# Kernel tuning notes

Hardware: AMD Instinct MI355X
Metric: run time of the kernel (lower is better)

The kernel has to match this reference:

```python
import jax, jax.numpy as jnp
import numpy as np
from itertools import product as iter_product

N_QUBITS = 6
DIM = 2 ** N_QUBITS            # 64
N_GEN = DIM * DIM - 1          # 4095
DEPTH = 4
N_OBS = 15

_GENS = None

def _build_generators(n):
    I = np.eye(2, dtype=np.complex64)
    X = np.array([[0, 1], [1, 0]], np.complex64)
    Y = np.array([[0, -1j], [1j, 0]], np.complex64)
    Z = np.array([[1, 0], [0, -1]], np.complex64)
    P = [I, X, Y, Z]
    gens = []
    for idx in iter_product(range(4), repeat=n):
        if all(i == 0 for i in idx):
            continue
        m = P[idx[0]]
        for k in range(1, n):
            m = np.kron(m, P[idx[k]])
        gens.append(m)
    return jnp.asarray(np.stack(gens))  # [4^n-1, 2^n, 2^n] complex64

def _gens():
    global _GENS
    if _GENS is None:
        _GENS = _build_generators(N_QUBITS)
    return _GENS

def _apply_ry(psi, q, theta, n):
    # psi: [B, 2^n] complex; RY(theta) on qubit q
    B = psi.shape[0]
    x = psi.reshape(B, 2 ** q, 2, 2 ** (n - q - 1))
    c = jnp.cos(theta / 2)
    s = jnp.sin(theta / 2)
    s0, s1 = x[:, :, 0, :], x[:, :, 1, :]
    x = jnp.stack([c * s0 - s * s1, s * s0 + c * s1], axis=2)
    return x.reshape(B, -1)

def _apply_cnot(psi, c, t, n):
    # psi: [B, 2^n]; CNOT control c, target t
    B = psi.shape[0]
    x = psi.reshape((B,) + (2,) * n)
    ax_c, ax_t = 1 + c, 1 + t
    x0 = jnp.take(x, 0, axis=ax_c)
    x1 = jnp.take(x, 1, axis=ax_c)
    ax_t2 = ax_t - (1 if ax_t > ax_c else 0)
    x1 = jnp.flip(x1, axis=ax_t2)
    x = jnp.stack([x0, x1], axis=ax_c)
    return x.reshape(B, -1)

def _make_hermitians(A, B, D):
    # create_Hermitian vectorized over the m observables.
    # h[i,j] = A[idx]+iB[idx] for j<i (row-major lower-tri), h[i-1,i-1]=D[i];
    # then H = h + h^H.
    il, jl = jnp.tril_indices(DIM, -1)  # row-major order matches count+j loop
    di = jnp.arange(DIM - 1)

    def one(a, b, d):
        h = jnp.zeros((DIM, DIM), jnp.complex64)
        h = h.at[il, jl].set(a + 1j * b)
        h = h.at[di, di].set(d[1:].astype(jnp.complex64))
        return h + h.conj().T

    return jax.vmap(one)(A, B, D)  # [m, DIM, DIM]

def setup_inputs() -> dict:
    key = jax.random.key(0)
    ks = jax.random.split(key, 8)
    batch, input_dim, hidden = 256, 1024, 2047
    n_off = DIM * (DIM - 1) // 2  # 2016
    return {
        "x": jax.random.normal(ks[0], (batch, input_dim), jnp.float32),
        "W1": 0.02 * jax.random.normal(ks[1], (input_dim, hidden), jnp.float32),
        "b1": jnp.zeros((hidden,), jnp.float32),
        "W2": 0.02 * jax.random.normal(ks[2], (hidden, N_GEN), jnp.float32),
        "b2": jnp.zeros((N_GEN,), jnp.float32),
        "var_params": 0.01 * jax.random.normal(ks[3], (DEPTH, N_QUBITS), jnp.float32),
        "A": 2.0 * jax.random.normal(ks[4], (N_OBS, n_off), jnp.float32),
        "B": 2.0 * jax.random.normal(ks[5], (N_OBS, n_off), jnp.float32),
        "D": 2.0 * jax.random.normal(ks[6], (N_OBS, DIM), jnp.float32),
    }

def reference(x, W1, b1, W2, b2, var_params, A, B, D):
    n = N_QUBITS
    # encoding projection: Linear -> SiLU -> Linear
    h = jax.nn.silu(x @ W1 + b1)
    theta = h @ W2 + b2  # [batch, 4^n - 1]
    gens = _gens()  # [n_gen, dim, dim] complex64 (constant)
    # A_mat = sum_g theta_g G_g (Hermitian), U = exp(i A_mat)
    Amat = jnp.einsum('bg,gij->bij', theta.astype(jnp.complex64), gens)
    U = jax.vmap(jax.scipy.linalg.expm)(1j * Amat)  # [batch, dim, dim]
    psi = U[:, :, 0]  # apply to |0...0>
    # hardware-efficient VQC: RY layer + CNOT ring per depth
    for d in range(DEPTH):
        for q in range(n):
            psi = _apply_ry(psi, q, var_params[d, q], n)
        for q in range(n):
            psi = _apply_cnot(psi, q, (q + 1) % n, n)
    H = _make_hermitians(A, B, D)  # [m, dim, dim]
    # expectation <psi|H_w|psi>
    exp = jnp.einsum('bi,wij,bj->bw', psi.conj(), H, psi).real
    return exp  # [batch, n_observables]
```

## Files before the change

### kernel.cpp

```cpp
#include <hip/hip_runtime.h>
#include <math.h>

typedef unsigned short ushort_t;
typedef __attribute__((ext_vector_type(8))) short bf16x8_t;
typedef __attribute__((ext_vector_type(4))) float f32x4_t;

__device__ __forceinline__ void tsplit(float v, unsigned& h, unsigned& l) {
  unsigned u = __float_as_uint(v);
  h = u >> 16;
  float lo = v - __uint_as_float(u & 0xffff0000u);
  l = __float_as_uint(lo) >> 16;
}

__device__ __forceinline__ void transpose_tile(
    const float* __restrict__ W, ushort_t* __restrict__ Wh,
    ushort_t* __restrict__ Wl, int K, int N, int Kpad, int n0, int k0, int t) {
  __shared__ float sh[32][33];
  const int tx = t & 31, ty = t >> 5;
#pragma unroll
  for (int i = 0; i < 4; ++i) {
    int k = k0 + i * 8 + ty;
    float v = (k < K && (n0 + tx) < N) ? W[(size_t)k * N + n0 + tx] : 0.f;
    sh[tx][i * 8 + ty] = v;
  }
  __syncthreads();
  const int nn = t >> 3;
  const int kq = t & 7;
  unsigned h[4], l[4];
#pragma unroll
  for (int e = 0; e < 4; ++e) tsplit(sh[nn][kq * 4 + e], h[e], l[e]);
  size_t o = (size_t)(n0 + nn) * Kpad + k0 + kq * 4;
  uint2 ph, pl;
  ph.x = h[0] | (h[1] << 16); ph.y = h[2] | (h[3] << 16);
  pl.x = l[0] | (l[1] << 16); pl.y = l[2] | (l[3] << 16);
  *(uint2*)&Wh[o] = ph;
  *(uint2*)&Wl[o] = pl;
}

__global__ __launch_bounds__(256) void prep2_kernel(
    const float* __restrict__ x, const float* __restrict__ W1,
    ushort_t* __restrict__ xh, ushort_t* __restrict__ xl,
    ushort_t* __restrict__ w1h, ushort_t* __restrict__ w1l) {
  const int bid = blockIdx.x;
  const int t = threadIdx.x;
  if (bid < 256) {
    int i4 = bid * 256 + t;
    float4 v = ((const float4*)x)[i4];
    unsigned h0, l0, h1, l1, h2, l2, h3, l3;
    tsplit(v.x, h0, l0); tsplit(v.y, h1, l1);
    tsplit(v.z, h2, l2); tsplit(v.w, h3, l3);
    uint2 ph, pl;
    ph.x = h0 | (h1 << 16); ph.y = h2 | (h3 << 16);
    pl.x = l0 | (l1 << 16); pl.y = l2 | (l3 << 16);
    ((uint2*)xh)[i4] = ph;
    ((uint2*)xl)[i4] = pl;
  } else {
    int tau = bid - 256;
    transpose_tile(W1, w1h, w1l, 1024, 2047, 1024,
                   (tau & 63) * 32, (tau >> 6) * 32, t);
  }
}

#define LSTR 40

__global__ __launch_bounds__(256) void gemm1_w2t_kernel(
    const ushort_t* __restrict__ xh, const ushort_t* __restrict__ xl,
    const ushort_t* __restrict__ w1h, const ushort_t* __restrict__ w1l,
    const float* __restrict__ b1,
    ushort_t* __restrict__ hh, ushort_t* __restrict__ hl,
    const float* __restrict__ W2,
    ushort_t* __restrict__ w2h, ushort_t* __restrict__ w2l) {
  const int bid = blockIdx.x;
  const int t = threadIdx.x;
  if (bid >= 256) {
    int tau = bid - 256;
    transpose_tile(W2, w2h, w2l, 2047, 4095, 2048,
                   (tau & 127) * 32, (tau >> 7) * 32, t);
    return;
  }
  __shared__ ushort_t As[2][32 * LSTR];
  __shared__ ushort_t Bs[2][64 * LSTR];
  const int lane = t & 63;
  const int wv = t >> 6;
  const int l15 = lane & 15;
  const int quad = lane >> 4;
  const int m0 = (bid >> 5) * 32;
  const int n0 = (bid & 31) * 64;

  f32x4_t acc[2];
  acc[0] = (f32x4_t){0.f, 0.f, 0.f, 0.f};
  acc[1] = (f32x4_t){0.f, 0.f, 0.f, 0.f};

  for (int k0 = 0; k0 < 1024; k0 += 32) {
    if (wv < 2) {
      const ushort_t* src = wv ? xl : xh;
      ushort_t* dst = As[wv];
#pragma unroll
      for (int q = 0; q < 2; ++q) {
        int r = q * 16 + (lane >> 2);
        int c = (lane & 3) * 8;
        *(int4*)&dst[r * LSTR + c] =
            *(const int4*)(src + (size_t)(m0 + r) * 1024 + k0 + c);
      }
    } else {
      const ushort_t* src = (wv == 3) ? w1l : w1h;
      ushort_t* dst = Bs[wv - 2];
#pragma unroll
      for (int q = 0; q < 4; ++q) {
        int r = q * 16 + (lane >> 2);
        int c = (lane & 3) * 8;
        *(int4*)&dst[r * LSTR + c] =
            *(const int4*)(src + (size_t)(n0 + r) * 1024 + k0 + c);
      }
    }
    __syncthreads();
    bf16x8_t bfh = *(const bf16x8_t*)&Bs[0][(wv * 16 + l15) * LSTR + quad * 8];
    bf16x8_t bfl = *(const bf16x8_t*)&Bs[1][(wv * 16 + l15) * LSTR + quad * 8];
#pragma unroll
    for (int i = 0; i < 2; ++i) {
      int mr = i * 16 + l15;
      bf16x8_t afh = *(const bf16x8_t*)&As[0][mr * LSTR + quad * 8];
      bf16x8_t afl = *(const bf16x8_t*)&As[1][mr * LSTR + quad * 8];
      acc[i] = __builtin_amdgcn_mfma_f32_16x16x32_bf16(afh, bfh, acc[i], 0, 0, 0);
      acc[i] = __builtin_amdgcn_mfma_f32_16x16x32_bf16(afh, bfl, acc[i], 0, 0, 0);
      acc[i] = __builtin_amdgcn_mfma_f32_16x16x32_bf16(afl, bfh, acc[i], 0, 0, 0);
    }
    __syncthreads();
  }
#pragma unroll
  for (int i = 0; i < 2; ++i) {
    int col = n0 + wv * 16 + l15;
#pragma unroll
    for (int rg = 0; rg < 4; ++rg) {
      int row = m0 + i * 16 + quad * 4 + rg;
      float v = acc[i][rg];
      if (col < 2047) {
        v += b1[col];
        v = v / (1.f + expf(-v));
      } else {
        v = 0.f;
      }
      unsigned h, l;
      tsplit(v, h, l);
      size_t o = (size_t)row * 2048 + col;
      hh[o] = (ushort_t)h;
      hl[o] = (ushort_t)l;
    }
  }
}

__global__ __launch_bounds__(256) void gemm2k_kernel(
    const ushort_t* __restrict__ Ah, const ushort_t* __restrict__ Al,
    const ushort_t* __restrict__ Bh, const ushort_t* __restrict__ Bl,
    float* __restrict__ part) {
  __shared__ ushort_t Ab[2][128 * LSTR];
  __shared__ ushort_t Bb[2][64 * LSTR];
  const int t = threadIdx.x;
  const int lane = t & 63;
  const int wv = t >> 6;
  const int l15 = lane & 15;
  const int quad = lane >> 4;
  const int wm = wv >> 1, wn = wv & 1;
  const int m0 = blockIdx.y * 128;
  const int n0 = blockIdx.x * 64;
  const int ks = blockIdx.z;

  f32x4_t acc[4][2];
#pragma unroll
  for (int i = 0; i < 4; ++i)
#pragma unroll
    for (int j = 0; j < 2; ++j) acc[i][j] = (f32x4_t){0.f, 0.f, 0.f, 0.f};

  for (int kt = 0; kt < 16; ++kt) {
    const int k0 = ks * 512 + kt * 32;
    if (wv < 2) {
      const ushort_t* src = wv ? Al : Ah;
      ushort_t* dst = Ab[wv];
#pragma unroll
      for (int q = 0; q < 8; ++q) {
        int r = q * 16 + (lane >> 2);
        int c = (lane & 3) * 8;
        *(int4*)&dst[r * LSTR + c] =
            *(const int4*)(src + (size_t)(m0 + r) * 2048 + k0 + c);
      }
    } else {
      const ushort_t* src = (wv == 3) ? Bl : Bh;
      ushort_t* dst = Bb[wv - 2];
#pragma unroll
      for (int q = 0; q < 4; ++q) {
        int r = q * 16 + (lane >> 2);
        int c = (lane & 3) * 8;
        *(int4*)&dst[r * LSTR + c] =
            *(const int4*)(src + (size_t)(n0 + r) * 2048 + k0 + c);
      }
    }
    __syncthreads();
    bf16x8_t bfh[2], bfl[2];
#pragma unroll
    for (int j = 0; j < 2; ++j) {
      int nr = wn * 32 + j * 16 + l15;
      bfh[j] = *(const bf16x8_t*)&Bb[0][nr * LSTR + quad * 8];
      bfl[j] = *(const bf16x8_t*)&Bb[1][nr * LSTR + quad * 8];
    }
#pragma unroll
    for (int i = 0; i < 4; ++i) {
      int mr = wm * 64 + i * 16 + l15;
      bf16x8_t afh = *(const bf16x8_t*)&Ab[0][mr * LSTR + quad * 8];
      bf16x8_t afl = *(const bf16x8_t*)&Ab[1][mr * LSTR + quad * 8];
#pragma unroll
      for (int j = 0; j < 2; ++j) {
        acc[i][j] = __builtin_amdgcn_mfma_f32_16x16x32_bf16(
            afh, bfh[j], acc[i][j], 0, 0, 0);
        acc[i][j] = __builtin_amdgcn_mfma_f32_16x16x32_bf16(
            afh, bfl[j], acc[i][j], 0, 0, 0);
        acc[i][j] = __builtin_amdgcn_mfma_f32_16x16x32_bf16(
            afl, bfh[j], acc[i][j], 0, 0, 0);
      }
    }
    __syncthreads();
  }
  float* pbase = part + (size_t)ks * 256 * 4096;
#pragma unroll
  for (int i = 0; i < 4; ++i)
#pragma unroll
    for (int j = 0; j < 2; ++j) {
      int row0 = m0 + wm * 64 + i * 16 + quad * 4;
      int col = n0 + wn * 32 + j * 16 + l15;
#pragma unroll
      for (int rg = 0; rg < 4; ++rg)
        pbase[(size_t)(row0 + rg) * 4096 + col] = acc[i][j][rg];
    }
}

#define TM 64
#define TN 64
#define TK 16
__global__ __launch_bounds__(256) void gemm_tiled(
    const float* __restrict__ X, const float* __restrict__ W,
    const float* __restrict__ bias, float* __restrict__ out,
    int M, int N, int K, int ldx, int ldw, int ldo, int doSilu, int padN)
{
  __shared__ float Xs[TK][TM + 4];
  __shared__ float Ws[TK][TN + 4];
  const int t = threadIdx.x;
  const int n0 = blockIdx.x * TN;
  const int m0 = blockIdx.y * TM;
  const int tr = t >> 4, tc = t & 15;
  float acc[4][4];
#pragma unroll
  for (int i = 0; i < 4; ++i)
#pragma unroll
    for (int j = 0; j < 4; ++j) acc[i][j] = 0.f;
  const int xr = t >> 2, xk = (t & 3) * 4;
  const int wk = t >> 4, wc = (t & 15) * 4;
  for (int k0 = 0; k0 < K; k0 += TK) {
    {
      const float* xp = X + (size_t)(m0 + xr) * ldx + (k0 + xk);
      float xv[4];
      if (k0 + xk + 3 < K) {
        float4 v = *(const float4*)xp;
        xv[0] = v.x; xv[1] = v.y; xv[2] = v.z; xv[3] = v.w;
      } else {
#pragma unroll
        for (int e = 0; e < 4; ++e) xv[e] = (k0 + xk + e < K) ? xp[e] : 0.f;
      }
#pragma unroll
      for (int e = 0; e < 4; ++e) Xs[xk + e][xr] = xv[e];
    }
    {
      const int kk = k0 + wk;
      const float* wp = W + (size_t)kk * ldw + (n0 + wc);
      const bool kv = kk < K;
#pragma unroll
      for (int e = 0; e < 4; ++e) {
        int n = n0 + wc + e;
        Ws[wk][wc + e] = (kv && n < N) ? wp[e] : 0.f;
      }
    }
    __syncthreads();
#pragma unroll
    for (int k = 0; k < TK; ++k) {
      float4 av = *(const float4*)&Xs[k][tr * 4];
      float4 bv = *(const float4*)&Ws[k][tc * 4];
      float a4[4] = {av.x, av.y, av.z, av.w};
      float b4[4] = {bv.x, bv.y, bv.z, bv.w};
#pragma unroll
      for (int i = 0; i < 4; ++i)
#pragma unroll
        for (int j = 0; j < 4; ++j)
          acc[i][j] = fmaf(a4[i], b4[j], acc[i][j]);
    }
    __syncthreads();
  }
#pragma unroll
  for (int i = 0; i < 4; ++i) {
    const int mrow = m0 + tr * 4 + i;
    float* op = out + (size_t)mrow * ldo;
#pragma unroll
    for (int j = 0; j < 4; ++j) {
      const int n = n0 + tc * 4 + j;
      if (n < N) {
        float v = acc[i][j] + bias[n];
        if (doSilu) v = v / (1.f + expf(-v));
        op[n] = v;
      } else if (n < padN) {
        op[n] = 0.f;
      }
    }
  }
}

#define RS 72
#define PL (64 * RS)

__device__ __forceinline__ void qmm4(
    const ushort_t* __restrict__ Prm, const ushort_t* __restrict__ Qcm,
    float* ore, float* oim, int mt, int nt, int quad, int l15)
{
  f32x4_t aR = (f32x4_t){0.f, 0.f, 0.f, 0.f};
  f32x4_t aN = (f32x4_t){0.f, 0.f, 0.f, 0.f};
  f32x4_t aI = (f32x4_t){0.f, 0.f, 0.f, 0.f};
#pragma unroll
  for (int kb = 0; kb < 2; ++kb) {
    const int ko = kb * 32 + quad * 8;
    const int ra = (mt * 16 + l15) * RS + ko;
    bf16x8_t arh = *(const bf16x8_t*)&Prm[0 * PL + ra];
    bf16x8_t arl = *(const bf16x8_t*)&Prm[1 * PL + ra];
    bf16x8_t aih = *(const bf16x8_t*)&Prm[2 * PL + ra];
    bf16x8_t ail = *(const bf16x8_t*)&Prm[3 * PL + ra];
    const int rb = (nt * 16 + l15) * RS + ko;
    bf16x8_t brh = *(const bf16x8_t*)&Qcm[0 * PL + rb];
    bf16x8_t brl = *(const bf16x8_t*)&Qcm[1 * PL + rb];
    bf16x8_t bih = *(const bf16x8_t*)&Qcm[2 * PL + rb];
    bf16x8_t bil = *(const bf16x8_t*)&Qcm[3 * PL + rb];
    aR = __builtin_amdgcn_mfma_f32_16x16x32_bf16(arh, brh, aR, 0, 0, 0);
    aR = __builtin_amdgcn_mfma_f32_16x16x32_bf16(arh, brl, aR, 0, 0, 0);
    aR = __builtin_amdgcn_mfma_f32_16x16x32_bf16(arl, brh, aR, 0, 0, 0);
    aN = __builtin_amdgcn_mfma_f32_16x16x32_bf16(aih, bih, aN, 0, 0, 0);
    aN = __builtin_amdgcn_mfma_f32_16x16x32_bf16(aih, bil, aN, 0, 0, 0);
    aN = __builtin_amdgcn_mfma_f32_16x16x32_bf16(ail, bih, aN, 0, 0, 0);
    aI = __builtin_amdgcn_mfma_f32_16x16x32_bf16(arh, bih, aI, 0, 0, 0);
    aI = __builtin_amdgcn_mfma_f32_16x16x32_bf16(arh, bil, aI, 0, 0, 0);
    aI = __builtin_amdgcn_mfma_f32_16x16x32_bf16(arl, bih, aI, 0, 0, 0);
    aI = __builtin_amdgcn_mfma_f32_16x16x32_bf16(aih, brh, aI, 0, 0, 0);
    aI = __builtin_amdgcn_mfma_f32_16x16x32_bf16(aih, brl, aI, 0, 0, 0);
    aI = __builtin_amdgcn_mfma_f32_16x16x32_bf16(ail, brh, aI, 0, 0, 0);
  }
#pragma unroll
  for (int rg = 0; rg < 4; ++rg) {
    ore[rg] = aR[rg] - aN[rg];
    oim[rg] = aI[rg];
  }
}

__device__ __forceinline__ void stage_rm4(
    ushort_t* rm, const float* re, const float* im, int mt, int nt,
    int quad, int l15)
{
  unsigned rh[4], rl[4], ih[4], il[4];
#pragma unroll
  for (int rg = 0; rg < 4; ++rg) {
    tsplit(re[rg], rh[rg], rl[rg]);
    tsplit(im[rg], ih[rg], il[rg]);
  }
#pragma unroll
  for (int rg = 0; rg < 4; ++rg) {
    int idx = (mt * 16 + quad * 4 + rg) * RS + nt * 16 + l15;
    rm[0 * PL + idx] = (ushort_t)rh[rg];
    rm[1 * PL + idx] = (ushort_t)rl[rg];
    rm[2 * PL + idx] = (ushort_t)ih[rg];
    rm[3 * PL + idx] = (ushort_t)il[rg];
  }
}

__device__ __forceinline__ void stage_cm4(
    ushort_t* cm, const float* re, const float* im, int mt, int nt,
    int quad, int l15)
{
  unsigned rh[4], rl[4], ih[4], il[4];
#pragma unroll
  for (int rg = 0; rg < 4; ++rg) {
    tsplit(re[rg], rh[rg], rl[rg]);
    tsplit(im[rg], ih[rg], il[rg]);
  }
  int base = (nt * 16 + l15) * RS + mt * 16 + quad * 4;
  uint2 p;
  p.x = rh[0] | (rh[1] << 16); p.y = rh[2] | (rh[3] << 16);
  *(uint2*)&cm[0 * PL + base] = p;
  p.x = rl[0] | (rl[1] << 16); p.y = rl[2] | (rl[3] << 16);
  *(uint2*)&cm[1 * PL + base] = p;
  p.x = ih[0] | (ih[1] << 16); p.y = ih[2] | (ih[3] << 16);
  *(uint2*)&cm[2 * PL + base] = p;
  p.x = il[0] | (il[1] << 16); p.y = il[2] | (il[3] << 16);
  *(uint2*)&cm[3 * PL + base] = p;
}

__device__ __forceinline__ void stage_both4(
    ushort_t* rm, ushort_t* cm, const float* re, const float* im,
    int mt, int nt, int quad, int l15)
{
  stage_rm4(rm, re, im, mt, nt, quad, l15);
  stage_cm4(cm, re, im, mt, nt, quad, l15);
}

__global__ __launch_bounds__(1024, 4) void quantum_kernel(
    const float* __restrict__ pin,
    const float* __restrict__ b2g,
    const float* __restrict__ vp,
    const float* __restrict__ Aobs,
    const float* __restrict__ Bobs,
    const float* __restrict__ Dobs,
    float* __restrict__ out,
    int fused)
{
  __shared__ __align__(16) ushort_t PQ[2][8 * PL];
  __shared__ float ps[128];
  __shared__ float scr16[16];
  __shared__ float csb[24], snb[24];
  __shared__ float sAf;
  __shared__ int   sS;

  float*  thetas = (float*)&PQ[1][0];
  float2* Als    = (float2*)&PQ[0][0];

  const int t = threadIdx.x;
  const int b = blockIdx.x;
  const int lane = t & 63;
  const int w = t >> 6;
  const int quad = lane >> 4;
  const int l15 = lane & 15;
  const int mt = w >> 2, nt = w & 3;

  float ssq;
  {
    float4 v = ((const float4*)(pin + (size_t)b * 4096))[t];
    if (fused) {
#pragma unroll
      for (int k = 1; k < 4; ++k) {
        float4 u =
            ((const float4*)(pin + (size_t)k * 256 * 4096 + (size_t)b * 4096))[t];
        v.x += u.x; v.y += u.y; v.z += u.z; v.w += u.w;
      }
      int n0i = 4 * t;
      v.x += b2g[n0i];
      v.y += b2g[n0i + 1];
      v.z += b2g[n0i + 2];
      if (n0i + 3 < 4095) v.w += b2g[n0i + 3];
    }
    if (t == 1023) v.w = 0.f;
    thetas[4 * t + 0] = v.x; thetas[4 * t + 1] = v.y;
    thetas[4 * t + 2] = v.z; thetas[4 * t + 3] = v.w;
    ssq = v.x * v.x + v.y * v.y + v.z * v.z + v.w * v.w;
  }
#pragma unroll
  for (int mm = 1; mm < 64; mm <<= 1) ssq += __shfl_xor(ssq, mm);
  if (lane == 0) scr16[w] = ssq;
  __syncthreads();
  if (w == 0) {
    float s = (lane < 16) ? scr16[lane] : 0.f;
#pragma unroll
    for (int mm = 1; mm < 64; mm <<= 1) s += __shfl_xor(s, mm);
    if (lane == 0) {
      float frob = fmaxf(8.f * sqrtf(s), 1e-3f);
      sAf = frob;
      float bound = 0.30f * frob;
      int sc = (bound > 1.f) ? (int)ceilf(log2f(bound)) : 0;
      sS = sc < 0 ? 0 : (sc > 12 ? 12 : sc);
    }
  } else if (w == 1 && lane < 24) {
    float sn, cs;
    sincosf(vp[lane] * 0.5f, &sn, &cs);
    snb[lane] = sn;
    csb[lane] = cs;
  }
  __syncthreads();
  const int sPow = sS;

  for (int xx = 0; xx < 4; ++xx) {
    const int x = w + 16 * xx;
    const int z = lane;
    int g1 = 0;
#pragma unroll
    for (int bq = 0; bq < 6; ++bq) {
      int xb = (x >> bq) & 1, zb = (z >> bq) & 1;
      int dig = xb ? (zb ? 2 : 1) : (zb ? 3 : 0);
      g1 |= dig << (2 * bq);
    }
    float tv = (g1 == 0) ? 0.f : thetas[g1 - 1];
    int pc = __popc(x & z) & 3;
    float re, im;
    switch (pc) {
      case 0:  re = tv;  im = 0.f;  break;
      case 1:  re = 0.f; im = -tv;  break;
      case 2:  re = -tv; im = 0.f;  break;
      default: re = 0.f; im = tv;   break;
    }
#pragma unroll
    for (int mk = 1; mk < 64; mk <<= 1) {
      float ore = __shfl_xor(re, mk);
      float oim = __shfl_xor(im, mk);
      if (z & mk) { re = ore - re; im = oim - im; }
      else        { re = re + ore; im = im + oim; }
    }
    Als[z * 66 + (z ^ x)] = make_float2(re, im);
  }
  __syncthreads();

  const float scl = ldexpf(1.f, -sPow);
  float bre[4], bim[4];
#pragma unroll
  for (int rg = 0; rg < 4; ++rg) {
    int row = mt * 16 + quad * 4 + rg;
    int col = nt * 16 + l15;
    float2 v = Als[row * 66 + col];
    bre[rg] = -v.y * scl;
    bim[rg] =  v.x * scl;
  }
  __syncthreads();

  ushort_t* b0 = &PQ[0][0];
  ushort_t* b1 = &PQ[1][0];
  stage_both4(b0, b0 + 4 * PL, bre, bim, mt, nt, quad, l15);
  __syncthreads();
  float b2re[4], b2im[4];
  qmm4(b0, b0 + 4 * PL, b2re, b2im, mt, nt, quad, l15);
  stage_both4(b1, b1 + 4 * PL, b2re, b2im, mt, nt, quad, l15);
  __syncthreads();
  float b3re[4], b3im[4];
  qmm4(b1, b0 + 4 * PL, b3re, b3im, mt, nt, quad, l15);

  const float c3 = 1.f / 6.f, c4 = 1.f / 24.f, c5 = 1.f / 120.f;
  const float c6 = 1.f / 720.f, c7 = 1.f / 5040.f, c8 = 1.f / 40320.f;
  float s1re[4], s1im[4], p0re[4], p0im[4];
#pragma unroll
  for (int rg = 0; rg < 4; ++rg) {
    float dg = (mt == nt && l15 == quad * 4 + rg) ? 1.f : 0.f;
    s1re[rg] = c4 * dg + c5 * bre[rg] + c6 * b2re[rg] + c7 * b3re[rg];
    s1im[rg] =           c5 * bim[rg] + c6 * b2im[rg] + c7 * b3im[rg];
    p0re[rg] = dg + bre[rg] + 0.5f * b2re[rg] + c3 * b3re[rg];
    p0im[rg] =      bim[rg] + 0.5f * b2im[rg] + c3 * b3im[rg];
  }
  float b4re[4], b4im[4];
  qmm4(b1, b1 + 4 * PL, b4re, b4im, mt, nt, quad, l15);
#pragma unroll
  for (int rg = 0; rg < 4; ++rg) {
    s1re[rg] += c8 * b4re[rg];
    s1im[rg] += c8 * b4im[rg];
  }
  __syncthreads();
  stage_rm4(b0, s1re, s1im, mt, nt, quad, l15);
  stage_cm4(b0 + 4 * PL, b4re, b4im, mt, nt, quad, l15);
  __syncthreads();
  float ure[4], uim[4];
  qmm4(b0, b0 + 4 * PL, ure, uim, mt, nt, quad, l15);
#pragma unroll
  for (int rg = 0; rg < 4; ++rg) {
    ure[rg] += p0re[rg];
    uim[rg] += p0im[rg];
  }

  int cur = 1;
  for (int q = 0; q < sPow; ++q) {
    ushort_t* bb = &PQ[cur][0];
    stage_both4(bb, bb + 4 * PL, ure, uim, mt, nt, quad, l15);
    __syncthreads();
    qmm4(bb, bb + 4 * PL, ure, uim, mt, nt, quad, l15);
    cur ^= 1;
  }

  if (nt == 0 && l15 == 0) {
#pragma unroll
    for (int rg = 0; rg < 4; ++rg) {
      int row = mt * 16 + quad * 4 + rg;
      ps[2 * row] = ure[rg];
      ps[2 * row + 1] = uim[rg];
    }
  }
  __syncthreads();

  if (t < 64) {
    float pre = ps[2 * t], pim = ps[2 * t + 1];
#pragma unroll
    for (int d = 0; d < 4; ++d) {
#pragma unroll
      for (int q = 0; q < 6; ++q) {
        float s = snb[d * 6 + q], c = csb[d * 6 + q];
        int bpos = 5 - q;
        int bit = (t >> bpos) & 1;
        float ore = __shfl_xor(pre, 1 << bpos);
        float oim = __shfl_xor(pim, 1 << bpos);
        float sg = bit ? s : -s;
        pre = c * pre + sg * ore;
        pim = c * pim + sg * oim;
      }
#pragma unroll
      for (int q = 0; q < 6; ++q) {
        int bc = 5 - q;
        int bt = 5 - ((q + 1) % 6);
        float ore = __shfl_xor(pre, 1 << bt);
        float oim = __shfl_xor(pim, 1 << bt);
        int ctrl = (t >> bc) & 1;
        pre = ctrl ? ore : pre;
        pim = ctrl ? oim : pim;
      }
    }
    ps[2 * t] = pre; ps[2 * t + 1] = pim;
  }
  __syncthreads();

  float* Rt = (float*)&PQ[0][0];
  float* It = Rt + 2016;
  for (int p = t; p < 2016; p += 1024) {
    int i = (int)((1.f + sqrtf(8.f * (float)p + 1.f)) * 0.5f);
    while (i * (i - 1) / 2 > p) --i;
    while (i * (i + 1) / 2 <= p) ++i;
    int j = p - i * (i - 1) / 2;
    float pri = ps[2 * i], pii = ps[2 * i + 1];
    float prj = ps[2 * j], pij = ps[2 * j + 1];
    Rt[p] = pri * prj + pii * pij;
    It[p] = pri * pij - pii * prj;
  }
  __syncthreads();

  if (w < 15) {
    float xr = ps[2 * lane], xi = ps[2 * lane + 1];
    float mypsq = xr * xr + xi * xi;
    const float* Ap = Aobs + w * 2016;
    const float* Bp = Bobs + w * 2016;
    float part = 0.f;
    for (int p2 = lane; p2 < 1008; p2 += 64) {
      float2 a = *(const float2*)&Ap[2 * p2];
      float2 bb2 = *(const float2*)&Bp[2 * p2];
      float2 rt = *(const float2*)&Rt[2 * p2];
      float2 it = *(const float2*)&It[2 * p2];
      part += a.x * rt.x - bb2.x * it.x;
      part += a.y * rt.y - bb2.y * it.y;
    }
    if (lane < 63) part += Dobs[w * 64 + lane + 1] * mypsq;
#pragma unroll
    for (int mm = 1; mm < 64; mm <<= 1) part += __shfl_xor(part, mm);
    if (lane == 0) out[b * 15 + w] = 2.f * part;
  }
}

extern "C" void kernel_launch(void* const* d_in, const int* in_sizes, int n_in,
                              void* d_out, int out_size, void* d_ws, size_t ws_size,
                              hipStream_t stream) {
  const float* x  = (const float*)d_in[0];
  const float* W1 = (const float*)d_in[1];
  const float* b1 = (const float*)d_in[2];
  const float* W2 = (const float*)d_in[3];
  const float* b2 = (const float*)d_in[4];
  const float* vp = (const float*)d_in[5];
  const float* Ao = (const float*)d_in[6];
  const float* Bo = (const float*)d_in[7];
  const float* Do = (const float*)d_in[8];
  float* out = (float*)d_out;

  const size_t O_XH  = 0;
  const size_t O_XL  = 524288;
  const size_t O_W1H = 1048576;
  const size_t O_W1L = 5242880;
  const size_t O_PT  = 0;
  const size_t O_W2H = 16777216;
  const size_t O_W2L = 33554432;
  const size_t O_HH  = 50331648;
  const size_t O_HL  = 51380224;
  const size_t NEED  = 52428800;

  if (ws_size >= NEED) {
    char* ws = (char*)d_ws;
    ushort_t* xh  = (ushort_t*)(ws + O_XH);
    ushort_t* xl  = (ushort_t*)(ws + O_XL);
    ushort_t* w1h = (ushort_t*)(ws + O_W1H);
    ushort_t* w1l = (ushort_t*)(ws + O_W1L);
    float* part16 = (float*)(ws + O_PT);
    ushort_t* w2h = (ushort_t*)(ws + O_W2H);
    ushort_t* w2l = (ushort_t*)(ws + O_W2L);
    ushort_t* hh  = (ushort_t*)(ws + O_HH);
    ushort_t* hl  = (ushort_t*)(ws + O_HL);

    prep2_kernel<<<2304, 256, 0, stream>>>(x, W1, xh, xl, w1h, w1l);
    gemm1_w2t_kernel<<<8448, 256, 0, stream>>>(
        xh, xl, w1h, w1l, b1, hh, hl, W2, w2h, w2l);
    gemm2k_kernel<<<dim3(64, 2, 4), 256, 0, stream>>>(hh, hl, w2h, w2l, part16);
    quantum_kernel<<<256, 1024, 0, stream>>>(part16, b2, vp, Ao, Bo, Do, out, 1);
  } else {
    float* h     = (float*)d_ws;
    float* theta = h + 256 * 2048;
    gemm_tiled<<<dim3(32, 4), 256, 0, stream>>>(
        x, W1, b1, h, 256, 2047, 1024, 1024, 2047, 2048, 1, 2048);
    gemm_tiled<<<dim3(64, 4), 256, 0, stream>>>(
        h, W2, b2, theta, 256, 4095, 2047, 2048, 4095, 4096, 0, 4096);
    quantum_kernel<<<256, 1024, 0, stream>>>(theta, b2, vp, Ao, Bo, Do, out, 0);
  }
}
```

Before: 173.9 us.

## Fuse fp32-to-bf16 hi/lo splitting into GEMM tile loads, drop prep transposes

The separate prep pass and the W2 transpose pass are removed. Both GEMMs now read fp32 x, W1 and W2 directly and split them into bf16 hi/lo pairs while staging tiles in shared memory. This cuts a kernel launch and the round trip of writing and re-reading large transposed weight copies in the workspace. In exchange, the weight loads in the GEMM loops become strided column reads (one float per thread per row), which may be poorly coalesced, and each gemm2 block repeats the split work that was previously done once.

```diff
diff --git a/kernel.cpp b/kernel.cpp
--- a/kernel.cpp
+++ b/kernel.cpp
@@ -12,149 +12,104 @@
   l = __float_as_uint(lo) >> 16;
 }
 
-__device__ __forceinline__ void transpose_tile(
-    const float* __restrict__ W, ushort_t* __restrict__ Wh,
-    ushort_t* __restrict__ Wl, int K, int N, int Kpad, int n0, int k0, int t) {
-  __shared__ float sh[32][33];
-  const int tx = t & 31, ty = t >> 5;
-#pragma unroll
-  for (int i = 0; i < 4; ++i) {
-    int k = k0 + i * 8 + ty;
-    float v = (k < K && (n0 + tx) < N) ? W[(size_t)k * N + n0 + tx] : 0.f;
-    sh[tx][i * 8 + ty] = v;
-  }
-  __syncthreads();
-  const int nn = t >> 3;
-  const int kq = t & 7;
-  unsigned h[4], l[4];
-#pragma unroll
-  for (int e = 0; e < 4; ++e) tsplit(sh[nn][kq * 4 + e], h[e], l[e]);
-  size_t o = (size_t)(n0 + nn) * Kpad + k0 + kq * 4;
-  uint2 ph, pl;
-  ph.x = h[0] | (h[1] << 16); ph.y = h[2] | (h[3] << 16);
-  pl.x = l[0] | (l[1] << 16); pl.y = l[2] | (l[3] << 16);
-  *(uint2*)&Wh[o] = ph;
-  *(uint2*)&Wl[o] = pl;
-}
-
-__global__ __launch_bounds__(256) void prep2_kernel(
+__device__ __forceinline__ void split8(const float* p, bf16x8_t& hi, bf16x8_t& lo) {
+#pragma unroll
+  for (int e = 0; e < 8; ++e) {
+    unsigned h, l;
+    tsplit(p[e], h, l);
+    hi[e] = (short)h;
+    lo[e] = (short)l;
+  }
+}
+
+#define LSTR 40
+
+__global__ __launch_bounds__(512) void gemm1_kernel(
     const float* __restrict__ x, const float* __restrict__ W1,
-    ushort_t* __restrict__ xh, ushort_t* __restrict__ xl,
-    ushort_t* __restrict__ w1h, ushort_t* __restrict__ w1l) {
-  const int bid = blockIdx.x;
+    const float* __restrict__ b1,
+    ushort_t* __restrict__ hh, ushort_t* __restrict__ hl) {
+  __shared__ __align__(16) ushort_t As[2][32 * LSTR];
+  __shared__ __align__(16) ushort_t Bs[2][64 * LSTR];
   const int t = threadIdx.x;
-  if (bid < 256) {
-    int i4 = bid * 256 + t;
-    float4 v = ((const float4*)x)[i4];
-    unsigned h0, l0, h1, l1, h2, l2, h3, l3;
-    tsplit(v.x, h0, l0); tsplit(v.y, h1, l1);
-    tsplit(v.z, h2, l2); tsplit(v.w, h3, l3);
-    uint2 ph, pl;
-    ph.x = h0 | (h1 << 16); ph.y = h2 | (h3 << 16);
-    pl.x = l0 | (l1 << 16); pl.y = l2 | (l3 << 16);
-    ((uint2*)xh)[i4] = ph;
-    ((uint2*)xl)[i4] = pl;
-  } else {
-    int tau = bid - 256;
-    transpose_tile(W1, w1h, w1l, 1024, 2047, 1024,
-                   (tau & 63) * 32, (tau >> 6) * 32, t);
-  }
-}
-
-#define LSTR 40
-
-__global__ __launch_bounds__(256) void gemm1_w2t_kernel(
-    const ushort_t* __restrict__ xh, const ushort_t* __restrict__ xl,
-    const ushort_t* __restrict__ w1h, const ushort_t* __restrict__ w1l,
-    const float* __restrict__ b1,
-    ushort_t* __restrict__ hh, ushort_t* __restrict__ hl,
-    const float* __restrict__ W2,
-    ushort_t* __restrict__ w2h, ushort_t* __restrict__ w2l) {
-  const int bid = blockIdx.x;
-  const int t = threadIdx.x;
-  if (bid >= 256) {
-    int tau = bid - 256;
-    transpose_tile(W2, w2h, w2l, 2047, 4095, 2048,
-                   (tau & 127) * 32, (tau >> 7) * 32, t);
-    return;
-  }
-  __shared__ ushort_t As[2][32 * LSTR];
-  __shared__ ushort_t Bs[2][64 * LSTR];
   const int lane = t & 63;
   const int wv = t >> 6;
   const int l15 = lane & 15;
   const int quad = lane >> 4;
-  const int m0 = (bid >> 5) * 32;
-  const int n0 = (bid & 31) * 64;
-
-  f32x4_t acc[2];
-  acc[0] = (f32x4_t){0.f, 0.f, 0.f, 0.f};
-  acc[1] = (f32x4_t){0.f, 0.f, 0.f, 0.f};
+  const int wm = wv & 1;
+  const int wn = wv >> 1;
+  const int m0 = (blockIdx.x >> 5) * 32;
+  const int n0 = (blockIdx.x & 31) * 64;
+
+  f32x4_t acc = (f32x4_t){0.f, 0.f, 0.f, 0.f};
+
+  const int xrow = (t & 127) >> 2;
+  const int xkq  = (t & 3) * 8;
+  const int wu   = t - 128;
+  const int wnx  = wu & 63;
+  const int wkh  = (wu >> 6) & 3;
+  const bool wok = (n0 + wnx) < 2047;
 
   for (int k0 = 0; k0 < 1024; k0 += 32) {
-    if (wv < 2) {
-      const ushort_t* src = wv ? xl : xh;
-      ushort_t* dst = As[wv];
-#pragma unroll
-      for (int q = 0; q < 2; ++q) {
-        int r = q * 16 + (lane >> 2);
-        int c = (lane & 3) * 8;
-        *(int4*)&dst[r * LSTR + c] =
-            *(const int4*)(src + (size_t)(m0 + r) * 1024 + k0 + c);
-      }
+    if (t < 128) {
+      const float* src = x + (size_t)(m0 + xrow) * 1024 + k0 + xkq;
+      float p[8];
+      float4 va = *(const float4*)src;
+      float4 vb = *(const float4*)(src + 4);
+      p[0] = va.x; p[1] = va.y; p[2] = va.z; p[3] = va.w;
+      p[4] = vb.x; p[5] = vb.y; p[6] = vb.z; p[7] = vb.w;
+      bf16x8_t hi, lo;
+      split8(p, hi, lo);
+      *(bf16x8_t*)&As[0][xrow * LSTR + xkq] = hi;
+      *(bf16x8_t*)&As[1][xrow * LSTR + xkq] = lo;
+    } else if (t < 384) {
+      float p[8];
+#pragma unroll
+      for (int i = 0; i < 8; ++i) {
+        int k = k0 + wkh * 8 + i;
+        p[i] = wok ? W1[(size_t)k * 2047 + n0 + wnx] : 0.f;
+      }
+      bf16x8_t hi, lo;
+      split8(p, hi, lo);
+      *(bf16x8_t*)&Bs[0][wnx * LSTR + wkh * 8] = hi;
+      *(bf16x8_t*)&Bs[1][wnx * LSTR + wkh * 8] = lo;
+    }
+    __syncthreads();
+    const int nr = wn * 16 + l15;
+    bf16x8_t bfh = *(const bf16x8_t*)&Bs[0][nr * LSTR + quad * 8];
+    bf16x8_t bfl = *(const bf16x8_t*)&Bs[1][nr * LSTR + quad * 8];
+    const int mr = wm * 16 + l15;
+    bf16x8_t afh = *(const bf16x8_t*)&As[0][mr * LSTR + quad * 8];
+    bf16x8_t afl = *(const bf16x8_t*)&As[1][mr * LSTR + quad * 8];
+    acc = __builtin_amdgcn_mfma_f32_16x16x32_bf16(afh, bfh, acc, 0, 0, 0);
+    acc = __builtin_amdgcn_mfma_f32_16x16x32_bf16(afh, bfl, acc, 0, 0, 0);
+    acc = __builtin_amdgcn_mfma_f32_16x16x32_bf16(afl, bfh, acc, 0, 0, 0);
+    __syncthreads();
+  }
+  const int col = n0 + wn * 16 + l15;
+#pragma unroll
+  for (int rg = 0; rg < 4; ++rg) {
+    int row = m0 + wm * 16 + quad * 4 + rg;
+    float v = acc[rg];
+    if (col < 2047) {
+      v += b1[col];
+      v = v / (1.f + expf(-v));
     } else {
-      const ushort_t* src = (wv == 3) ? w1l : w1h;
-      ushort_t* dst = Bs[wv - 2];
-#pragma unroll
-      for (int q = 0; q < 4; ++q) {
-        int r = q * 16 + (lane >> 2);
-        int c = (lane & 3) * 8;
-        *(int4*)&dst[r * LSTR + c] =
-            *(const int4*)(src + (size_t)(n0 + r) * 1024 + k0 + c);
-      }
-    }
-    __syncthreads();
-    bf16x8_t bfh = *(const bf16x8_t*)&Bs[0][(wv * 16 + l15) * LSTR + quad * 8];
-    bf16x8_t bfl = *(const bf16x8_t*)&Bs[1][(wv * 16 + l15) * LSTR + quad * 8];
-#pragma unroll
-    for (int i = 0; i < 2; ++i) {
-      int mr = i * 16 + l15;
-      bf16x8_t afh = *(const bf16x8_t*)&As[0][mr * LSTR + quad * 8];
-      bf16x8_t afl = *(const bf16x8_t*)&As[1][mr * LSTR + quad * 8];
-      acc[i] = __builtin_amdgcn_mfma_f32_16x16x32_bf16(afh, bfh, acc[i], 0, 0, 0);
-      acc[i] = __builtin_amdgcn_mfma_f32_16x16x32_bf16(afh, bfl, acc[i], 0, 0, 0);
-      acc[i] = __builtin_amdgcn_mfma_f32_16x16x32_bf16(afl, bfh, acc[i], 0, 0, 0);
-    }
-    __syncthreads();
-  }
-#pragma unroll
-  for (int i = 0; i < 2; ++i) {
-    int col = n0 + wv * 16 + l15;
-#pragma unroll
-    for (int rg = 0; rg < 4; ++rg) {
-      int row = m0 + i * 16 + quad * 4 + rg;
-      float v = acc[i][rg];
-      if (col < 2047) {
-        v += b1[col];
-        v = v / (1.f + expf(-v));
-      } else {
-        v = 0.f;
-      }
-      unsigned h, l;
-      tsplit(v, h, l);
-      size_t o = (size_t)row * 2048 + col;
-      hh[o] = (ushort_t)h;
-      hl[o] = (ushort_t)l;
-    }
+      v = 0.f;
+    }
+    unsigned h, l;
+    tsplit(v, h, l);
+    size_t o = (size_t)row * 2048 + col;
+    hh[o] = (ushort_t)h;
+    hl[o] = (ushort_t)l;
   }
 }
 
 __global__ __launch_bounds__(256) void gemm2k_kernel(
     const ushort_t* __restrict__ Ah, const ushort_t* __restrict__ Al,
-    const ushort_t* __restrict__ Bh, const ushort_t* __restrict__ Bl,
+    const float* __restrict__ W2,
     float* __restrict__ part) {
-  __shared__ ushort_t Ab[2][128 * LSTR];
-  __shared__ ushort_t Bb[2][64 * LSTR];
+  __shared__ __align__(16) ushort_t Ab[2][128 * LSTR];
+  __shared__ __align__(16) ushort_t Bb[2][64 * LSTR];
   const int t = threadIdx.x;
   const int lane = t & 63;
   const int wv = t >> 6;
@@ -165,6 +120,11 @@
   const int n0 = blockIdx.x * 64;
   const int ks = blockIdx.z;
 
+  const int wu  = t - 128;
+  const int bn  = wu & 63;
+  const int bkh = (wu >> 6) & 1;
+  const bool bok = (n0 + bn) < 4095;
+
   f32x4_t acc[4][2];
 #pragma unroll
   for (int i = 0; i < 4; ++i)
@@ -184,14 +144,18 @@
             *(const int4*)(src + (size_t)(m0 + r) * 2048 + k0 + c);
       }
     } else {
-      const ushort_t* src = (wv == 3) ? Bl : Bh;
-      ushort_t* dst = Bb[wv - 2];
-#pragma unroll
-      for (int q = 0; q < 4; ++q) {
-        int r = q * 16 + (lane >> 2);
-        int c = (lane & 3) * 8;
-        *(int4*)&dst[r * LSTR + c] =
-            *(const int4*)(src + (size_t)(n0 + r) * 2048 + k0 + c);
+      float p[16];
+#pragma unroll
+      for (int i = 0; i < 16; ++i) {
+        int k = k0 + bkh * 16 + i;
+        p[i] = (bok && k < 2047) ? W2[(size_t)k * 4095 + n0 + bn] : 0.f;
+      }
+#pragma unroll
+      for (int half = 0; half < 2; ++half) {
+        bf16x8_t hi, lo;
+        split8(&p[half * 8], hi, lo);
+        *(bf16x8_t*)&Bb[0][bn * LSTR + bkh * 16 + half * 8] = hi;
+        *(bf16x8_t*)&Bb[1][bn * LSTR + bkh * 16 + half * 8] = lo;
       }
     }
     __syncthreads();
@@ -657,33 +621,19 @@
   const float* Do = (const float*)d_in[8];
   float* out = (float*)d_out;
 
-  const size_t O_XH  = 0;
-  const size_t O_XL  = 524288;
-  const size_t O_W1H = 1048576;
-  const size_t O_W1L = 5242880;
-  const size_t O_PT  = 0;
-  const size_t O_W2H = 16777216;
-  const size_t O_W2L = 33554432;
-  const size_t O_HH  = 50331648;
-  const size_t O_HL  = 51380224;
-  const size_t NEED  = 52428800;
+  const size_t O_PT = 0;
+  const size_t O_HH = 16777216;
+  const size_t O_HL = 17825792;
+  const size_t NEED = 18874368;
 
   if (ws_size >= NEED) {
     char* ws = (char*)d_ws;
-    ushort_t* xh  = (ushort_t*)(ws + O_XH);
-    ushort_t* xl  = (ushort_t*)(ws + O_XL);
-    ushort_t* w1h = (ushort_t*)(ws + O_W1H);
-    ushort_t* w1l = (ushort_t*)(ws + O_W1L);
     float* part16 = (float*)(ws + O_PT);
-    ushort_t* w2h = (ushort_t*)(ws + O_W2H);
-    ushort_t* w2l = (ushort_t*)(ws + O_W2L);
     ushort_t* hh  = (ushort_t*)(ws + O_HH);
     ushort_t* hl  = (ushort_t*)(ws + O_HL);
 
-    prep2_kernel<<<2304, 256, 0, stream>>>(x, W1, xh, xl, w1h, w1l);
-    gemm1_w2t_kernel<<<8448, 256, 0, stream>>>(
-        xh, xl, w1h, w1l, b1, hh, hl, W2, w2h, w2l);
-    gemm2k_kernel<<<dim3(64, 2, 4), 256, 0, stream>>>(hh, hl, w2h, w2l, part16);
+    gemm1_kernel<<<256, 512, 0, stream>>>(x, W1, b1, hh, hl);
+    gemm2k_kernel<<<dim3(64, 2, 4), 256, 0, stream>>>(hh, hl, W2, part16);
     quantum_kernel<<<256, 1024, 0, stream>>>(part16, b2, vp, Ao, Bo, Do, out, 1);
   } else {
     float* h     = (float*)d_ws;
```

Result: no change. 176.6 us (+1.5%).
